# Kernel optimization log

Hardware: AMD Instinct MI355X
Metric: run time of the kernel (lower is better)

The kernel has to match this reference:

```python
import jax, jax.numpy as jnp
import numpy as np

B, M, P, A, T = 32, 128, 20, 32, 32
H = 32   # embed_size / local hidden
E = 64   # local_hidden_dim = 2*H, global attention embed dim


def setup_inputs() -> dict:
    key = jax.random.key(0)
    ks = jax.random.split(key, 10)
    def w(k, shape, fan):
        return jax.random.normal(k, shape, jnp.float32) / np.float32(np.sqrt(fan))
    z = lambda *s: jnp.zeros(s, jnp.float32)
    o = lambda *s: jnp.ones(s, jnp.float32)
    return {
        "map_states": jax.random.normal(ks[0], (B, M, P, 16), jnp.float32),
        "agent_states": jax.random.normal(ks[1], (B, A, T, 4), jnp.float32),
        "m_W1": w(ks[2], (16, H), 16), "m_b1": z(H), "m_g1": o(H), "m_be1": z(H),
        "m_W2": w(ks[3], (H, H), H),   "m_b2": z(H), "m_g2": o(H), "m_be2": z(H),
        "a_W1": w(ks[4], (4, H), 4),   "a_b1": z(H), "a_g1": o(H), "a_be1": z(H),
        "a_W2": w(ks[5], (H, H), H),   "a_b2": z(H), "a_g2": o(H), "a_be2": z(H),
        # stacked attention params: index 0 = a2m, 1 = agent(self), 2 = m2a
        "att_Wq": w(ks[6], (3, E, E), E), "att_bq": z(3, E),
        "att_Wk": w(ks[7], (3, E, E), E), "att_bk": z(3, E),
        "att_Wv": w(ks[8], (3, E, E), E), "att_bv": z(3, E),
        "att_Wo": w(ks[9], (3, E, E), E), "att_bo": z(3, E),
    }


def _mlp(x, W, b, g, be):
    # Linear -> LayerNorm -> ReLU
    h = x @ W + b
    mu = jnp.mean(h, axis=-1, keepdims=True)
    var = jnp.var(h, axis=-1, keepdims=True)
    h = (h - mu) / jnp.sqrt(var + 1e-5) * g + be
    return jax.nn.relu(h)


def _local_graph(x, p1, p2):
    # x: [B, N, P, F] -> [B, N, 2H]
    e = _mlp(_mlp(x, *p1), *p2)                       # [B,N,P,H]
    n = e.shape[2]
    # faithful "max excluding self": max_j (e[j] - 10000*[j==i])
    mask = -10000.0 * jnp.eye(n, dtype=e.dtype)       # [Pi,Pj]
    nb = jnp.max(e[:, :, None, :, :] + mask[None, None, :, :, None], axis=3)  # [B,N,P,H]
    e = jnp.concatenate([e, nb], axis=-1)             # [B,N,P,2H]
    return jnp.max(e, axis=2)                          # [B,N,2H]


def _mha(q, k, v, Wq, bq, Wk, bk, Wv, bv, Wo, bo):
    # single-head attention, batch_first
    d = q.shape[-1]
    Q = q @ Wq + bq
    K = k @ Wk + bk
    V = v @ Wv + bv
    scores = jnp.einsum('bqd,bkd->bqk', Q, K) / jnp.sqrt(jnp.asarray(d, Q.dtype))
    attn = jax.nn.softmax(scores, axis=-1)
    return jnp.einsum('bqk,bkd->bqd', attn, V) @ Wo + bo


def reference(map_states, agent_states,
              m_W1, m_b1, m_g1, m_be1, m_W2, m_b2, m_g2, m_be2,
              a_W1, a_b1, a_g1, a_be1, a_W2, a_b2, a_g2, a_be2,
              att_Wq, att_bq, att_Wk, att_bk, att_Wv, att_bv, att_Wo, att_bo):
    map_emb = _local_graph(map_states, (m_W1, m_b1, m_g1, m_be1), (m_W2, m_b2, m_g2, m_be2))      # [B,M,E]
    agent_emb = _local_graph(agent_states, (a_W1, a_b1, a_g1, a_be1), (a_W2, a_b2, a_g2, a_be2))  # [B,A,E]

    target = agent_emb[:, :1]                                       # [B,1,E]
    kv = jnp.concatenate([target, map_emb], axis=1)                 # [B,M+1,E]
    a2m = _mha(map_emb, kv, kv, att_Wq[0], att_bq[0], att_Wk[0], att_bk[0],
               att_Wv[0], att_bv[0], att_Wo[0], att_bo[0])
    map_emb = map_emb + a2m
    t_a = _mha(target, target, target, att_Wq[1], att_bq[1], att_Wk[1], att_bk[1],
               att_Wv[1], att_bv[1], att_Wo[1], att_bo[1])
    t_m2a = _mha(target, map_emb, map_emb, att_Wq[2], att_bq[2], att_Wk[2], att_bk[2],
                 att_Wv[2], att_bv[2], att_Wo[2], att_bo[2])
    target = t_a + t_m2a                                            # [B,1,E]
    # pack (target_agent_embedding, map_embedding) into one array [B, M+1, E]
    return jnp.concatenate([target, map_emb], axis=1)
```

## Files before the change

### kernel.cpp

```cpp
#include <hip/hip_runtime.h>

#define BB 32
#define MM 128
#define PP 20
#define AA 32
#define TT 32
#define HH 32
#define EE 64

__device__ __forceinline__ float4 matvec64(const float* __restrict__ W,
                                           const float* __restrict__ xrow,
                                           int s, int t)
{
    const float4* __restrict__ Wv = (const float4*)W;
    const float4* __restrict__ xv = (const float4*)xrow;
    float4 acc = make_float4(0.f, 0.f, 0.f, 0.f);
#pragma unroll
    for (int ii = 0; ii < 4; ++ii) {
        const float4 xx = xv[s * 4 + ii];
        const int ib = s * 16 + ii * 4;
        const float4 w0 = Wv[(ib + 0) * 16 + t];
        const float4 w1 = Wv[(ib + 1) * 16 + t];
        const float4 w2 = Wv[(ib + 2) * 16 + t];
        const float4 w3 = Wv[(ib + 3) * 16 + t];
        acc.x = fmaf(xx.x, w0.x, acc.x); acc.y = fmaf(xx.x, w0.y, acc.y);
        acc.z = fmaf(xx.x, w0.z, acc.z); acc.w = fmaf(xx.x, w0.w, acc.w);
        acc.x = fmaf(xx.y, w1.x, acc.x); acc.y = fmaf(xx.y, w1.y, acc.y);
        acc.z = fmaf(xx.y, w1.z, acc.z); acc.w = fmaf(xx.y, w1.w, acc.w);
        acc.x = fmaf(xx.z, w2.x, acc.x); acc.y = fmaf(xx.z, w2.y, acc.y);
        acc.z = fmaf(xx.z, w2.z, acc.z); acc.w = fmaf(xx.z, w2.w, acc.w);
        acc.x = fmaf(xx.w, w3.x, acc.x); acc.y = fmaf(xx.w, w3.y, acc.y);
        acc.z = fmaf(xx.w, w3.z, acc.z); acc.w = fmaf(xx.w, w3.w, acc.w);
    }
    acc.x += __shfl_xor(acc.x, 16); acc.y += __shfl_xor(acc.y, 16);
    acc.z += __shfl_xor(acc.z, 16); acc.w += __shfl_xor(acc.w, 16);
    acc.x += __shfl_xor(acc.x, 32); acc.y += __shfl_xor(acc.y, 32);
    acc.z += __shfl_xor(acc.z, 32); acc.w += __shfl_xor(acc.w, 32);
    return acc;
}

template <int IN, int P>
__device__ __forceinline__ void lg_qkv_body(const float* __restrict__ xg,
                                            const float* __restrict__ W1, const float* __restrict__ b1,
                                            const float* __restrict__ g1, const float* __restrict__ be1,
                                            const float* __restrict__ W2, const float* __restrict__ b2,
                                            const float* __restrict__ g2, const float* __restrict__ be2,
                                            float* __restrict__ embRow,
                                            const float* __restrict__ Wq, const float* __restrict__ bq,
                                            const float* __restrict__ Wk, const float* __restrict__ bk,
                                            const float* __restrict__ Wv, const float* __restrict__ bv,
                                            float* __restrict__ Qrow,
                                            float* __restrict__ Krow,
                                            float* __restrict__ Vrow)
{
    constexpr int NPASS = (P + 7) / 8;
    const int tid  = threadIdx.x;
    const int wave = tid >> 6;
    const int lane = tid & 63;
    const int sub  = tid >> 5;
    const int c    = tid & 31;

    __shared__ __align__(16) float aslot[8][32];
    __shared__ __align__(16) float wmax[4][32];
    __shared__ __align__(16) float xrow[EE];

    float4 xr[NPASS][IN / 4];
#pragma unroll
    for (int ps = 0; ps < NPASS; ++ps) {
        int p = ps * 8 + sub;
        if (p > P - 1) p = P - 1;
        const float4* xp4 = (const float4*)(xg + (long)p * IN);
#pragma unroll
        for (int j = 0; j < IN / 4; ++j) xr[ps][j] = xp4[j];
    }

    float w1c[IN];
#pragma unroll
    for (int k = 0; k < IN; ++k) w1c[k] = W1[k * HH + c];
    float w2c[HH];
#pragma unroll
    for (int k = 0; k < HH; ++k) w2c[k] = W2[k * HH + c];
    const float b1c = b1[c], g1c = g1[c], be1c = be1[c];
    const float b2c = b2[c], g2c = g2[c], be2c = be2[c];

    float cmax = -1e30f;

#pragma unroll
    for (int ps = 0; ps < NPASS; ++ps) {
        const bool valid = (ps * 8 + sub) < P;

        float ha = b1c, hb = 0.0f;
#pragma unroll
        for (int j = 0; j < IN / 4; ++j) {
            const float4 xx = xr[ps][j];
            ha = fmaf(xx.x, w1c[4 * j + 0], ha);
            hb = fmaf(xx.y, w1c[4 * j + 1], hb);
            ha = fmaf(xx.z, w1c[4 * j + 2], ha);
            hb = fmaf(xx.w, w1c[4 * j + 3], hb);
        }
        const float h = ha + hb;

        float s1 = h, s2 = h * h;
#pragma unroll
        for (int off = 16; off >= 1; off >>= 1) {
            s1 += __shfl_xor(s1, off, 32);
            s2 += __shfl_xor(s2, off, 32);
        }
        const float mu  = s1 * (1.0f / 32.0f);
        float var = s2 * (1.0f / 32.0f) - mu * mu;
        var = fmaxf(var, 0.0f);
        float a = (h - mu) * rsqrtf(var + 1e-5f) * g1c + be1c;
        a = fmaxf(a, 0.0f);

        aslot[sub][c] = a;
        const float4* av4 = (const float4*)aslot[sub];
        float h2a = b2c, h2b = 0.0f;
#pragma unroll
        for (int j = 0; j < 8; ++j) {
            const float4 aa = av4[j];
            h2a = fmaf(aa.x, w2c[4 * j + 0], h2a);
            h2b = fmaf(aa.y, w2c[4 * j + 1], h2b);
            h2a = fmaf(aa.z, w2c[4 * j + 2], h2a);
            h2b = fmaf(aa.w, w2c[4 * j + 3], h2b);
        }
        const float h2 = h2a + h2b;

        float t1 = h2, t2 = h2 * h2;
#pragma unroll
        for (int off = 16; off >= 1; off >>= 1) {
            t1 += __shfl_xor(t1, off, 32);
            t2 += __shfl_xor(t2, off, 32);
        }
        const float mu2  = t1 * (1.0f / 32.0f);
        float var2 = t2 * (1.0f / 32.0f) - mu2 * mu2;
        var2 = fmaxf(var2, 0.0f);
        float e = (h2 - mu2) * rsqrtf(var2 + 1e-5f) * g2c + be2c;
        e = fmaxf(e, 0.0f);

        if (valid) cmax = fmaxf(cmax, e);
    }

    cmax = fmaxf(cmax, __shfl_xor(cmax, 32));
    if (lane < 32) wmax[wave][lane] = cmax;
    __syncthreads();

    if (tid < 32) {
        float fin = fmaxf(fmaxf(wmax[0][tid], wmax[1][tid]),
                          fmaxf(wmax[2][tid], wmax[3][tid]));
        xrow[tid]      = fin;
        xrow[tid + 32] = fin;
        embRow[tid]      = fin;
        embRow[tid + 32] = fin;
    }
    __syncthreads();

    const int s = lane >> 4, t = lane & 15;
    if (wave == 0) {
        if (Qrow) {
            float4 q4 = matvec64(Wq, xrow, s, t);
            if (s == 0) {
                const float4 bq4 = ((const float4*)bq)[t];
                float4 qo;
                qo.x = (q4.x + bq4.x) * 0.125f;
                qo.y = (q4.y + bq4.y) * 0.125f;
                qo.z = (q4.z + bq4.z) * 0.125f;
                qo.w = (q4.w + bq4.w) * 0.125f;
                ((float4*)Qrow)[t] = qo;
            }
        }
    } else if (wave == 1) {
        float4 k4 = matvec64(Wk, xrow, s, t);
        if (s == 0) {
            const float4 kb4 = ((const float4*)bk)[t];
            float4 ko;
            ko.x = k4.x + kb4.x; ko.y = k4.y + kb4.y;
            ko.z = k4.z + kb4.z; ko.w = k4.w + kb4.w;
            ((float4*)Krow)[t] = ko;
        }
    } else if (wave == 2) {
        float4 v4 = matvec64(Wv, xrow, s, t);
        if (s == 0) {
            const float4 vb4 = ((const float4*)bv)[t];
            float4 vo;
            vo.x = v4.x + vb4.x; vo.y = v4.y + vb4.y;
            vo.z = v4.z + vb4.z; vo.w = v4.w + vb4.w;
            ((float4*)Vrow)[t] = vo;
        }
    }
}

__global__ __launch_bounds__(256) void lg_qkv_kernel(
                              const float* __restrict__ map_states,
                              const float* __restrict__ agent_states,
                              const float* __restrict__ mW1, const float* __restrict__ mb1,
                              const float* __restrict__ mg1, const float* __restrict__ mbe1,
                              const float* __restrict__ mW2, const float* __restrict__ mb2,
                              const float* __restrict__ mg2, const float* __restrict__ mbe2,
                              const float* __restrict__ aW1, const float* __restrict__ ab1,
                              const float* __restrict__ ag1, const float* __restrict__ abe1,
                              const float* __restrict__ aW2, const float* __restrict__ ab2,
                              const float* __restrict__ ag2, const float* __restrict__ abe2,
                              const float* __restrict__ Wq, const float* __restrict__ bq,
                              const float* __restrict__ Wk, const float* __restrict__ bk,
                              const float* __restrict__ Wv, const float* __restrict__ bv,
                              float* __restrict__ map_emb,
                              float* __restrict__ target,
                              float* __restrict__ Qb,
                              float* __restrict__ Kb,
                              float* __restrict__ Vb)
{
    const int g = blockIdx.x;
    if (g < BB * MM) {
        const int b = g >> 7, m = g & 127;
        lg_qkv_body<16, PP>(map_states + (long)g * PP * 16,
                        mW1, mb1, mg1, mbe1, mW2, mb2, mg2, mbe2,
                        map_emb + (long)g * EE,
                        Wq, bq, Wk, bk, Wv, bv,
                        Qb + (long)g * EE,
                        Kb + ((long)b * 129 + 1 + m) * EE,
                        Vb + ((long)b * 129 + 1 + m) * EE);
    } else {
        const int b = g - BB * MM;
        lg_qkv_body<4, TT>(agent_states + (long)b * AA * TT * 4,
                       aW1, ab1, ag1, abe1, aW2, ab2, ag2, abe2,
                       target + (long)b * EE,
                       Wq, bq, Wk, bk, Wv, bv,
                       nullptr,
                       Kb + (long)b * 129 * EE,
                       Vb + (long)b * 129 * EE);
    }
}

__global__ void attn_fused_kernel(const float* __restrict__ map_emb,
                                  const float* __restrict__ Qb,
                                  const float* __restrict__ Kb,
                                  const float* __restrict__ Vb,
                                  const float* __restrict__ Wo, const float* __restrict__ bo,
                                  float* __restrict__ out)
{
    const int blk  = blockIdx.x;
    const int b    = blk >> 7;
    const int q    = blk & 127;
    const int lane = threadIdx.x;
    const int s = lane >> 4, t = lane & 15;

    __shared__ __align__(16) float sc[132];
    __shared__ __align__(16) float av[EE];

    const float4 q4 = ((const float4*)(Qb + ((long)b * MM + q) * EE))[t];

    const float* Kbase = Kb + (long)b * 129 * EE;
    float mx = -1e30f;
#pragma unroll 4
    for (int it = 0; it < 33; ++it) {
        const int j = it * 4 + s;
        const bool valid = (j < 129);
        float p = 0.0f;
        if (valid) {
            const float4 k4 = ((const float4*)(Kbase + (long)j * EE))[t];
            p = q4.x * k4.x + q4.y * k4.y + q4.z * k4.z + q4.w * k4.w;
        }
        p += __shfl_xor(p, 1); p += __shfl_xor(p, 2);
        p += __shfl_xor(p, 4); p += __shfl_xor(p, 8);
        if (valid) {
            mx = fmaxf(mx, p);
            if (t == 0) sc[j] = p;
        }
    }
#pragma unroll
    for (int off = 32; off >= 1; off >>= 1) mx = fmaxf(mx, __shfl_xor(mx, off));
    __syncthreads();

    float sum = 0.0f;
    for (int j = lane; j < 129; j += 64) {
        const float e = __expf(sc[j] - mx);
        sc[j] = e;
        sum += e;
    }
#pragma unroll
    for (int off = 32; off >= 1; off >>= 1) sum += __shfl_xor(sum, off);
    const float inv = 1.0f / sum;
    __syncthreads();

    const float* Vbase = Vb + (long)b * 129 * EE;
    float4 a4 = make_float4(0.f, 0.f, 0.f, 0.f);
#pragma unroll 4
    for (int it = 0; it < 33; ++it) {
        const int j = it * 4 + s;
        if (j < 129) {
            const float w = sc[j];
            const float4 v4 = ((const float4*)(Vbase + (long)j * EE))[t];
            a4.x = fmaf(w, v4.x, a4.x); a4.y = fmaf(w, v4.y, a4.y);
            a4.z = fmaf(w, v4.z, a4.z); a4.w = fmaf(w, v4.w, a4.w);
        }
    }
    a4.x += __shfl_xor(a4.x, 16); a4.y += __shfl_xor(a4.y, 16);
    a4.z += __shfl_xor(a4.z, 16); a4.w += __shfl_xor(a4.w, 16);
    a4.x += __shfl_xor(a4.x, 32); a4.y += __shfl_xor(a4.y, 32);
    a4.z += __shfl_xor(a4.z, 32); a4.w += __shfl_xor(a4.w, 32);
    if (s == 0) {
        float4 o; o.x = a4.x * inv; o.y = a4.y * inv; o.z = a4.z * inv; o.w = a4.w * inv;
        ((float4*)av)[t] = o;
    }
    __syncthreads();

    const float4 o4 = matvec64(Wo, av, s, t);
    if (s == 0) {
        const float4 bo4 = ((const float4*)bo)[t];
        const float4 x4 = ((const float4*)(map_emb + ((long)b * MM + q) * EE))[t];
        float4 res;
        res.x = o4.x + bo4.x + x4.x;
        res.y = o4.y + bo4.y + x4.y;
        res.z = o4.z + bo4.z + x4.z;
        res.w = o4.w + bo4.w + x4.w;
        ((float4*)(out + ((long)b * 129 + 1 + q) * EE))[t] = res;
    }
}

__global__ void target_kernel(const float* __restrict__ target,
                              const float* __restrict__ Wq2, const float* __restrict__ bq2,
                              const float* __restrict__ Wk2,
                              const float* __restrict__ Wv2, const float* __restrict__ bv2,
                              const float* __restrict__ Wo2, const float* __restrict__ bo2,
                              const float* __restrict__ Wv1, const float* __restrict__ bv1,
                              const float* __restrict__ Wo1, const float* __restrict__ bo1,
                              float* __restrict__ out)
{
    const int b    = blockIdx.x;
    const int lane = threadIdx.x;
    const int s = lane >> 4, t = lane & 15;

    __shared__ __align__(16) float trow[EE];
    __shared__ __align__(16) float tmp[EE];
    __shared__ __align__(16) float qtl[EE];
    __shared__ __align__(16) float qkl[EE];
    __shared__ __align__(16) float sc[128];
    __shared__ __align__(16) float av[EE];

    trow[lane] = target[(long)b * EE + lane];
    __syncthreads();

    const float4 v1 = matvec64(Wv1, trow, s, t);
    if (s == 0) {
        const float4 bv4 = ((const float4*)bv1)[t];
        float4 w; w.x = v1.x + bv4.x; w.y = v1.y + bv4.y; w.z = v1.z + bv4.z; w.w = v1.w + bv4.w;
        ((float4*)tmp)[t] = w;
    }
    __syncthreads();
    float4 ta = matvec64(Wo1, tmp, s, t);
    {
        const float4 bo4 = ((const float4*)bo1)[t];
        ta.x += bo4.x; ta.y += bo4.y; ta.z += bo4.z; ta.w += bo4.w;
    }

    float4 q4 = matvec64(Wq2, trow, s, t);
    if (s == 0) {
        const float4 bq4 = ((const float4*)bq2)[t];
        float4 qo;
        qo.x = (q4.x + bq4.x) * 0.125f;
        qo.y = (q4.y + bq4.y) * 0.125f;
        qo.z = (q4.z + bq4.z) * 0.125f;
        qo.w = (q4.w + bq4.w) * 0.125f;
        ((float4*)qtl)[t] = qo;
    }
    __syncthreads();

    {
        const float4* Wrow = (const float4*)(Wk2 + (long)lane * EE);
        const float4* qt4  = (const float4*)qtl;
        float qa = 0.f, qb = 0.f;
#pragma unroll
        for (int j = 0; j < 16; j += 2) {
            const float4 w0 = Wrow[j],     x0 = qt4[j];
            const float4 w1 = Wrow[j + 1], x1 = qt4[j + 1];
            qa = fmaf(w0.x, x0.x, qa); qb = fmaf(w0.y, x0.y, qb);
            qa = fmaf(w0.z, x0.z, qa); qb = fmaf(w0.w, x0.w, qb);
            qa = fmaf(w1.x, x1.x, qa); qb = fmaf(w1.y, x1.y, qb);
            qa = fmaf(w1.z, x1.z, qa); qb = fmaf(w1.w, x1.w, qb);
        }
        qkl[lane] = qa + qb;
    }
    __syncthreads();

    const float* Rbase = out + ((long)b * 129 + 1) * EE;
    const float4 qk4 = ((const float4*)qkl)[t];
    float mx = -1e30f;
#pragma unroll 4
    for (int it = 0; it < 32; ++it) {
        const int j = it * 4 + s;
        const float4 r4 = ((const float4*)(Rbase + (long)j * EE))[t];
        float p = qk4.x * r4.x + qk4.y * r4.y + qk4.z * r4.z + qk4.w * r4.w;
        p += __shfl_xor(p, 1); p += __shfl_xor(p, 2);
        p += __shfl_xor(p, 4); p += __shfl_xor(p, 8);
        mx = fmaxf(mx, p);
        if (t == 0) sc[j] = p;
    }
#pragma unroll
    for (int off = 32; off >= 1; off >>= 1) mx = fmaxf(mx, __shfl_xor(mx, off));
    __syncthreads();

    float sum = 0.0f;
#pragma unroll
    for (int j = lane; j < MM; j += 64) {
        const float e = __expf(sc[j] - mx);
        sc[j] = e;
        sum += e;
    }
#pragma unroll
    for (int off = 32; off >= 1; off >>= 1) sum += __shfl_xor(sum, off);
    const float inv = 1.0f / sum;
    __syncthreads();

    float4 b4 = make_float4(0.f, 0.f, 0.f, 0.f);
#pragma unroll 4
    for (int it = 0; it < 32; ++it) {
        const int j = it * 4 + s;
        const float w = sc[j];
        const float4 rr = ((const float4*)(Rbase + (long)j * EE))[t];
        b4.x = fmaf(w, rr.x, b4.x); b4.y = fmaf(w, rr.y, b4.y);
        b4.z = fmaf(w, rr.z, b4.z); b4.w = fmaf(w, rr.w, b4.w);
    }
    b4.x += __shfl_xor(b4.x, 16); b4.y += __shfl_xor(b4.y, 16);
    b4.z += __shfl_xor(b4.z, 16); b4.w += __shfl_xor(b4.w, 16);
    b4.x += __shfl_xor(b4.x, 32); b4.y += __shfl_xor(b4.y, 32);
    b4.z += __shfl_xor(b4.z, 32); b4.w += __shfl_xor(b4.w, 32);
    if (s == 0) {
        float4 o; o.x = b4.x * inv; o.y = b4.y * inv; o.z = b4.z * inv; o.w = b4.w * inv;
        ((float4*)av)[t] = o;
    }
    __syncthreads();

    const float4 vv = matvec64(Wv2, av, s, t);
    if (s == 0) {
        const float4 bv4 = ((const float4*)bv2)[t];
        float4 w; w.x = vv.x + bv4.x; w.y = vv.y + bv4.y; w.z = vv.z + bv4.z; w.w = vv.w + bv4.w;
        ((float4*)tmp)[t] = w;
    }
    __syncthreads();

    const float4 o4 = matvec64(Wo2, tmp, s, t);
    if (s == 0) {
        const float4 bo4 = ((const float4*)bo2)[t];
        float4 r;
        r.x = ta.x + o4.x + bo4.x;
        r.y = ta.y + o4.y + bo4.y;
        r.z = ta.z + o4.z + bo4.z;
        r.w = ta.w + o4.w + bo4.w;
        ((float4*)(out + (long)b * 129 * EE))[t] = r;
    }
}

extern "C" void kernel_launch(void* const* d_in, const int* in_sizes, int n_in,
                              void* d_out, int out_size, void* d_ws, size_t ws_size,
                              hipStream_t stream)
{
    const float* map_states   = (const float*)d_in[0];
    const float* agent_states = (const float*)d_in[1];
    const float* m_W1 = (const float*)d_in[2];
    const float* m_b1 = (const float*)d_in[3];
    const float* m_g1 = (const float*)d_in[4];
    const float* m_be1 = (const float*)d_in[5];
    const float* m_W2 = (const float*)d_in[6];
    const float* m_b2 = (const float*)d_in[7];
    const float* m_g2 = (const float*)d_in[8];
    const float* m_be2 = (const float*)d_in[9];
    const float* a_W1 = (const float*)d_in[10];
    const float* a_b1 = (const float*)d_in[11];
    const float* a_g1 = (const float*)d_in[12];
    const float* a_be1 = (const float*)d_in[13];
    const float* a_W2 = (const float*)d_in[14];
    const float* a_b2 = (const float*)d_in[15];
    const float* a_g2 = (const float*)d_in[16];
    const float* a_be2 = (const float*)d_in[17];
    const float* att_Wq = (const float*)d_in[18];
    const float* att_bq = (const float*)d_in[19];
    const float* att_Wk = (const float*)d_in[20];
    const float* att_bk = (const float*)d_in[21];
    const float* att_Wv = (const float*)d_in[22];
    const float* att_bv = (const float*)d_in[23];
    const float* att_Wo = (const float*)d_in[24];
    const float* att_bo = (const float*)d_in[25];

    float* out = (float*)d_out;

    float* ws      = (float*)d_ws;
    float* map_emb = ws;
    float* target  = map_emb + BB * MM * EE;
    float* Qb      = target + BB * EE;
    float* Kb      = Qb + BB * MM * EE;
    float* Vb      = Kb + BB * 129 * EE;

    const float* Wq0 = att_Wq + 0 * EE * EE; const float* bq0 = att_bq + 0 * EE;
    const float* Wk0 = att_Wk + 0 * EE * EE; const float* bk0 = att_bk + 0 * EE;
    const float* Wv0 = att_Wv + 0 * EE * EE; const float* bv0 = att_bv + 0 * EE;
    const float* Wo0 = att_Wo + 0 * EE * EE; const float* bo0 = att_bo + 0 * EE;
    const float* Wv1 = att_Wv + 1 * EE * EE; const float* bv1 = att_bv + 1 * EE;
    const float* Wo1 = att_Wo + 1 * EE * EE; const float* bo1 = att_bo + 1 * EE;
    const float* Wq2 = att_Wq + 2 * EE * EE; const float* bq2 = att_bq + 2 * EE;
    const float* Wk2 = att_Wk + 2 * EE * EE;
    const float* Wv2 = att_Wv + 2 * EE * EE; const float* bv2 = att_bv + 2 * EE;
    const float* Wo2 = att_Wo + 2 * EE * EE; const float* bo2 = att_bo + 2 * EE;

    hipLaunchKernelGGL(lg_qkv_kernel, dim3(BB * MM + BB), dim3(256), 0, stream,
                       map_states, agent_states,
                       m_W1, m_b1, m_g1, m_be1, m_W2, m_b2, m_g2, m_be2,
                       a_W1, a_b1, a_g1, a_be1, a_W2, a_b2, a_g2, a_be2,
                       Wq0, bq0, Wk0, bk0, Wv0, bv0,
                       map_emb, target, Qb, Kb, Vb);

    hipLaunchKernelGGL(attn_fused_kernel, dim3(BB * MM), dim3(64), 0, stream,
                       map_emb, Qb, Kb, Vb, Wo0, bo0, out);

    hipLaunchKernelGGL(target_kernel, dim3(BB), dim3(64), 0, stream,
                       target, Wq2, bq2, Wk2, Wv2, bv2, Wo2, bo2,
                       Wv1, bv1, Wo1, bo1, out);
}
```

Measured before the change: 176.1 us.

## Use online softmax in attention and widen local-graph block to 320 threads

The attention kernel now computes scores, runs an online softmax and accumulates V in one pass, then merges partial states across sub-groups with shuffles. This removes the shared-memory score buffer, two barriers and the separate second pass over K/V. The local-graph kernel moves from 8 to 10 sub-groups (320 threads), so the 20 points per row take two passes instead of three. The cost is extra exp calls per key in the online softmax and a larger block size, which may lower occupancy.

```diff
diff --git a/kernel.cpp b/kernel.cpp
--- a/kernel.cpp
+++ b/kernel.cpp
@@ -53,21 +53,22 @@
                                             float* __restrict__ Krow,
                                             float* __restrict__ Vrow)
 {
-    constexpr int NPASS = (P + 7) / 8;
+    constexpr int NSUB  = 10;
+    constexpr int NPASS = (P + NSUB - 1) / NSUB;
     const int tid  = threadIdx.x;
     const int wave = tid >> 6;
     const int lane = tid & 63;
     const int sub  = tid >> 5;
     const int c    = tid & 31;
 
-    __shared__ __align__(16) float aslot[8][32];
-    __shared__ __align__(16) float wmax[4][32];
+    __shared__ __align__(16) float aslot[NSUB][32];
+    __shared__ __align__(16) float wmax[5][32];
     __shared__ __align__(16) float xrow[EE];
 
     float4 xr[NPASS][IN / 4];
 #pragma unroll
     for (int ps = 0; ps < NPASS; ++ps) {
-        int p = ps * 8 + sub;
+        int p = ps * NSUB + sub;
         if (p > P - 1) p = P - 1;
         const float4* xp4 = (const float4*)(xg + (long)p * IN);
 #pragma unroll
@@ -87,7 +88,7 @@
 
 #pragma unroll
     for (int ps = 0; ps < NPASS; ++ps) {
-        const bool valid = (ps * 8 + sub) < P;
+        const bool valid = (ps * NSUB + sub) < P;
 
         float ha = b1c, hb = 0.0f;
 #pragma unroll
@@ -145,8 +146,9 @@
     __syncthreads();
 
     if (tid < 32) {
-        float fin = fmaxf(fmaxf(wmax[0][tid], wmax[1][tid]),
-                          fmaxf(wmax[2][tid], wmax[3][tid]));
+        float fin = fmaxf(fmaxf(fmaxf(wmax[0][tid], wmax[1][tid]),
+                                fmaxf(wmax[2][tid], wmax[3][tid])),
+                          wmax[4][tid]);
         xrow[tid]      = fin;
         xrow[tid + 32] = fin;
         embRow[tid]      = fin;
@@ -189,7 +191,7 @@
     }
 }
 
-__global__ __launch_bounds__(256) void lg_qkv_kernel(
+__global__ __launch_bounds__(320) void lg_qkv_kernel(
                               const float* __restrict__ map_states,
                               const float* __restrict__ agent_states,
                               const float* __restrict__ mW1, const float* __restrict__ mb1,
@@ -244,62 +246,61 @@
     const int lane = threadIdx.x;
     const int s = lane >> 4, t = lane & 15;
 
-    __shared__ __align__(16) float sc[132];
     __shared__ __align__(16) float av[EE];
 
     const float4 q4 = ((const float4*)(Qb + ((long)b * MM + q) * EE))[t];
 
     const float* Kbase = Kb + (long)b * 129 * EE;
-    float mx = -1e30f;
-#pragma unroll 4
-    for (int it = 0; it < 33; ++it) {
-        const int j = it * 4 + s;
-        const bool valid = (j < 129);
-        float p = 0.0f;
-        if (valid) {
-            const float4 k4 = ((const float4*)(Kbase + (long)j * EE))[t];
-            p = q4.x * k4.x + q4.y * k4.y + q4.z * k4.z + q4.w * k4.w;
-        }
-        p += __shfl_xor(p, 1); p += __shfl_xor(p, 2);
-        p += __shfl_xor(p, 4); p += __shfl_xor(p, 8);
-        if (valid) {
-            mx = fmaxf(mx, p);
-            if (t == 0) sc[j] = p;
-        }
-    }
-#pragma unroll
-    for (int off = 32; off >= 1; off >>= 1) mx = fmaxf(mx, __shfl_xor(mx, off));
-    __syncthreads();
-
-    float sum = 0.0f;
-    for (int j = lane; j < 129; j += 64) {
-        const float e = __expf(sc[j] - mx);
-        sc[j] = e;
-        sum += e;
-    }
-#pragma unroll
-    for (int off = 32; off >= 1; off >>= 1) sum += __shfl_xor(sum, off);
-    const float inv = 1.0f / sum;
-    __syncthreads();
-
     const float* Vbase = Vb + (long)b * 129 * EE;
-    float4 a4 = make_float4(0.f, 0.f, 0.f, 0.f);
+
+    float m = -1e30f, l = 0.0f;
+    float4 vacc = make_float4(0.f, 0.f, 0.f, 0.f);
+
 #pragma unroll 4
     for (int it = 0; it < 33; ++it) {
         const int j = it * 4 + s;
         if (j < 129) {
-            const float w = sc[j];
+            const float4 k4 = ((const float4*)(Kbase + (long)j * EE))[t];
+            float p = q4.x * k4.x + q4.y * k4.y + q4.z * k4.z + q4.w * k4.w;
+            p += __shfl_xor(p, 1); p += __shfl_xor(p, 2);
+            p += __shfl_xor(p, 4); p += __shfl_xor(p, 8);
             const float4 v4 = ((const float4*)(Vbase + (long)j * EE))[t];
-            a4.x = fmaf(w, v4.x, a4.x); a4.y = fmaf(w, v4.y, a4.y);
-            a4.z = fmaf(w, v4.z, a4.z); a4.w = fmaf(w, v4.w, a4.w);
-        }
-    }
-    a4.x += __shfl_xor(a4.x, 16); a4.y += __shfl_xor(a4.y, 16);
-    a4.z += __shfl_xor(a4.z, 16); a4.w += __shfl_xor(a4.w, 16);
-    a4.x += __shfl_xor(a4.x, 32); a4.y += __shfl_xor(a4.y, 32);
-    a4.z += __shfl_xor(a4.z, 32); a4.w += __shfl_xor(a4.w, 32);
-    if (s == 0) {
-        float4 o; o.x = a4.x * inv; o.y = a4.y * inv; o.z = a4.z * inv; o.w = a4.w * inv;
+            const float mn    = fmaxf(m, p);
+            const float alpha = __expf(m - mn);
+            const float e     = __expf(p - mn);
+            l = l * alpha + e;
+            vacc.x = fmaf(e, v4.x, vacc.x * alpha);
+            vacc.y = fmaf(e, v4.y, vacc.y * alpha);
+            vacc.z = fmaf(e, v4.z, vacc.z * alpha);
+            vacc.w = fmaf(e, v4.w, vacc.w * alpha);
+            m = mn;
+        }
+    }
+
+#pragma unroll
+    for (int off = 16; off <= 32; off <<= 1) {
+        const float mo = __shfl_xor(m, off);
+        const float lo = __shfl_xor(l, off);
+        float4 vo;
+        vo.x = __shfl_xor(vacc.x, off);
+        vo.y = __shfl_xor(vacc.y, off);
+        vo.z = __shfl_xor(vacc.z, off);
+        vo.w = __shfl_xor(vacc.w, off);
+        const float mn = fmaxf(m, mo);
+        const float a  = __expf(m - mn);
+        const float bb = __expf(mo - mn);
+        l = l * a + lo * bb;
+        vacc.x = vacc.x * a + vo.x * bb;
+        vacc.y = vacc.y * a + vo.y * bb;
+        vacc.z = vacc.z * a + vo.z * bb;
+        vacc.w = vacc.w * a + vo.w * bb;
+        m = mn;
+    }
+    const float inv = 1.0f / l;
+    if (s == 0) {
+        float4 o;
+        o.x = vacc.x * inv; o.y = vacc.y * inv;
+        o.z = vacc.z * inv; o.w = vacc.w * inv;
         ((float4*)av)[t] = o;
     }
     __syncthreads();
@@ -501,7 +502,7 @@
     const float* Wv2 = att_Wv + 2 * EE * EE; const float* bv2 = att_bv + 2 * EE;
     const float* Wo2 = att_Wo + 2 * EE * EE; const float* bo2 = att_bo + 2 * EE;
 
-    hipLaunchKernelGGL(lg_qkv_kernel, dim3(BB * MM + BB), dim3(256), 0, stream,
+    hipLaunchKernelGGL(lg_qkv_kernel, dim3(BB * MM + BB), dim3(320), 0, stream,
                        map_states, agent_states,
                        m_W1, m_b1, m_g1, m_be1, m_W2, m_b2, m_g2, m_be2,
                        a_W1, a_b1, a_g1, a_be1, a_W2, a_b2, a_g2, a_be2,
```

New measurement: 175.3 us. Within noise of the previous version (-0.4%).
